# Kernel optimization log

Measured on AMD Instinct MI355X. Metric: run time of the kernel, lower is better.

The kernel has to match this reference:

```python
import jax, jax.numpy as jnp
import numpy as np

NEG_INF = -1e9

def setup_inputs() -> dict:
    key = jax.random.key(0)
    ks = jax.random.split(key, 6)
    B, M, RNN, H, D = 64, 1024, 1024, 512, 2048
    return {
        "h": jax.random.normal(ks[0], (B, RNN), dtype=jnp.float32),
        "att_feats": jax.random.normal(ks[1], (B, M, D), dtype=jnp.float32),
        "att_mask": jax.random.randint(ks[2], (B, M), 0, 2, dtype=jnp.int32),
        "p_att_feats": jax.random.normal(ks[3], (B, M, H), dtype=jnp.float32),
        "W_ah": jax.random.normal(ks[4], (H, RNN), dtype=jnp.float32) * (1.0 / np.sqrt(RNN)),
        "w_alpha": jax.random.normal(ks[5], (H,), dtype=jnp.float32) * (1.0 / np.sqrt(H)),
    }

def reference(h, att_feats, att_mask, p_att_feats, W_ah, w_alpha):
    # Wah(h): [B, H]
    wah = h @ W_ah.T
    # additive attention energies: tanh(Wah(h)[:, None, :] + p_att_feats) -> [B, M, H]
    e = jnp.tanh(wah[:, None, :] + p_att_feats)
    # project to scalar per region: [B, M]
    logits = jnp.einsum("bmh,h->bm", e, w_alpha)
    logits = jnp.where(att_mask == 0, NEG_INF, logits)
    alpha = jax.nn.softmax(logits, axis=-1)
    # weighted sum of region features: [B, D]
    att = jnp.einsum("bm,bmd->bd", alpha, att_feats)
    return att
```

## Files before the change

### kernel.cpp

```cpp
#include <hip/hip_runtime.h>
#include <math.h>

#define B   64
#define M   1024
#define RNN 1024
#define H   512
#define D   2048
#define NEG_INF -1e9f

__device__ __forceinline__ float fast_tanh(float x) {
    float ax = fabsf(x);
    float t  = __expf(-2.0f * ax);
    float r  = (1.0f - t) * __builtin_amdgcn_rcpf(1.0f + t);
    return copysignf(r, x);
}

__global__ __launch_bounds__(256) void k_wah(const float* __restrict__ h,
                                             const float* __restrict__ W,
                                             float* __restrict__ wah) {
    int wid  = (blockIdx.x * 256 + threadIdx.x) >> 6;
    int lane = threadIdx.x & 63;
    int b = wid >> 9;
    int j = wid & (H - 1);
    const float4* hp = (const float4*)(h + (size_t)b * RNN);
    const float4* wp = (const float4*)(W + (size_t)j * RNN);
    float acc = 0.0f;
#pragma unroll
    for (int t = 0; t < 4; ++t) {
        int i = lane + t * 64;
        float4 a = hp[i];
        float4 w = wp[i];
        acc += a.x * w.x + a.y * w.y + a.z * w.z + a.w * w.w;
    }
#pragma unroll
    for (int off = 32; off > 0; off >>= 1)
        acc += __shfl_down(acc, off);
    if (lane == 0) wah[wid] = acc;
}

__global__ __launch_bounds__(256) void k_logits(const float* __restrict__ wah,
                                                const float* __restrict__ p_att,
                                                const int* __restrict__ mask,
                                                const float* __restrict__ w_alpha,
                                                float* __restrict__ logits) {
    int row  = (blockIdx.x * 256 + threadIdx.x) >> 6;
    int lane = threadIdx.x & 63;
    int b = row >> 10;
    if (mask[row] == 0) {
        if (lane == 0) logits[row] = NEG_INF;
        return;
    }
    const float4* pp  = (const float4*)(p_att + (size_t)row * H);
    const float4* whp = (const float4*)(wah + (size_t)b * H);
    const float4* wap = (const float4*)w_alpha;
    float acc = 0.0f;
#pragma unroll
    for (int t = 0; t < 2; ++t) {
        int i = lane + t * 64;
        float4 p  = pp[i];
        float4 wh = whp[i];
        float4 wa = wap[i];
        acc += fast_tanh(p.x + wh.x) * wa.x;
        acc += fast_tanh(p.y + wh.y) * wa.y;
        acc += fast_tanh(p.z + wh.z) * wa.z;
        acc += fast_tanh(p.w + wh.w) * wa.w;
    }
#pragma unroll
    for (int off = 32; off > 0; off >>= 1)
        acc += __shfl_down(acc, off);
    if (lane == 0) logits[row] = acc;
}

__global__ __launch_bounds__(256) void k_prep(const float* __restrict__ logits,
                                              uint2* __restrict__ ent,
                                              int* __restrict__ cnt) {
    const int b = blockIdx.x, tid = threadIdx.x;
    const int lane = tid & 63, wid = tid >> 6;
    __shared__ float s_al[M];
    __shared__ float s_red[4];
    __shared__ int   s_wcnt[16];
    __shared__ int   s_base[17];

    const float4* lg = (const float4*)(logits + (size_t)b * M);
    float4 v = lg[tid];
    float mx = fmaxf(fmaxf(v.x, v.y), fmaxf(v.z, v.w));
#pragma unroll
    for (int off = 32; off > 0; off >>= 1)
        mx = fmaxf(mx, __shfl_xor(mx, off));
    if (lane == 0) s_red[wid] = mx;
    __syncthreads();
    mx = fmaxf(fmaxf(s_red[0], s_red[1]), fmaxf(s_red[2], s_red[3]));

    float e0 = __expf(v.x - mx), e1 = __expf(v.y - mx);
    float e2 = __expf(v.z - mx), e3 = __expf(v.w - mx);
    float se = e0 + e1 + e2 + e3;
#pragma unroll
    for (int off = 32; off > 0; off >>= 1)
        se += __shfl_xor(se, off);
    __syncthreads();
    if (lane == 0) s_red[wid] = se;
    __syncthreads();
    const float inv = 1.0f / (s_red[0] + s_red[1] + s_red[2] + s_red[3]);

    float4 av = {e0 * inv, e1 * inv, e2 * inv, e3 * inv};
    ((float4*)s_al)[tid] = av;
    __syncthreads();

#pragma unroll
    for (int p = 0; p < 4; ++p) {
        float a = s_al[p * 256 + tid];
        unsigned long long bal = __ballot(a != 0.0f);
        if (lane == 0) s_wcnt[p * 4 + wid] = __popcll(bal);
    }
    __syncthreads();
    if (tid == 0) {
        int run = 0;
#pragma unroll
        for (int i = 0; i < 16; ++i) { s_base[i] = run; run += s_wcnt[i]; }
        s_base[16] = run;
        cnt[b] = (run + 15) & ~15;
    }
    __syncthreads();

    uint2* eb = ent + (size_t)b * M;
#pragma unroll
    for (int p = 0; p < 4; ++p) {
        int m = p * 256 + tid;
        float a = s_al[m];
        unsigned long long bal = __ballot(a != 0.0f);
        int pos = __popcll(bal & ((1ull << lane) - 1ull));
        if (a != 0.0f)
            eb[s_base[p * 4 + wid] + pos] =
                make_uint2((unsigned)(m * D * 4), __float_as_uint(a));
    }
    int total = s_base[16];
    int padded = (total + 15) & ~15;
    if (tid < 16 && total + tid < padded)
        eb[total + tid] = make_uint2(0u, 0u);
}

__global__ __launch_bounds__(128) void k_att(const uint2* __restrict__ ent,
                                             const int* __restrict__ cnt,
                                             const float* __restrict__ feats,
                                             float* __restrict__ out) {
    const int b = blockIdx.x, dq = blockIdx.y;
    const int tid = threadIdx.x;
    const int d0 = dq * 512 + tid * 4;
    const char* fbase = (const char*)(feats + (size_t)b * M * D + d0);
    const uint2* eb = ent + (size_t)b * M;
    const int n = cnt[b];

    float4 acc[4];
#pragma unroll
    for (int c = 0; c < 4; ++c) acc[c] = make_float4(0.f, 0.f, 0.f, 0.f);

    for (int i = 0; i < n; i += 16) {
        uint2 e[16];
#pragma unroll
        for (int u = 0; u < 16; ++u) e[u] = eb[i + u];
        float4 f[16];
#pragma unroll
        for (int u = 0; u < 16; ++u)
            f[u] = *(const float4*)(fbase + e[u].x);
#pragma unroll
        for (int u = 0; u < 16; ++u) {
            float a = __uint_as_float(e[u].y);
            float4 F = f[u];
            int c = u & 3;
            acc[c].x += a * F.x; acc[c].y += a * F.y;
            acc[c].z += a * F.z; acc[c].w += a * F.w;
        }
    }
    float4 r;
    r.x = (acc[0].x + acc[1].x) + (acc[2].x + acc[3].x);
    r.y = (acc[0].y + acc[1].y) + (acc[2].y + acc[3].y);
    r.z = (acc[0].z + acc[1].z) + (acc[2].z + acc[3].z);
    r.w = (acc[0].w + acc[1].w) + (acc[2].w + acc[3].w);
    *(float4*)(out + (size_t)b * D + d0) = r;
}

extern "C" void kernel_launch(void* const* d_in, const int* in_sizes, int n_in,
                              void* d_out, int out_size, void* d_ws, size_t ws_size,
                              hipStream_t stream) {
    const float* h       = (const float*)d_in[0];
    const float* feats   = (const float*)d_in[1];
    const int*   mask    = (const int*)d_in[2];
    const float* p_att   = (const float*)d_in[3];
    const float* W_ah    = (const float*)d_in[4];
    const float* w_alpha = (const float*)d_in[5];
    float* out = (float*)d_out;

    float* ws     = (float*)d_ws;
    float* wah    = ws;
    float* logits = wah + B * H;
    uint2* ent    = (uint2*)(logits + B * M);
    int*   cnt    = (int*)(ent + B * M);

    k_wah   <<<dim3(B * H / 4), 256, 0, stream>>>(h, W_ah, wah);
    k_logits<<<dim3(B * M / 4), 256, 0, stream>>>(wah, p_att, mask, w_alpha, logits);
    k_prep  <<<dim3(B), 256, 0, stream>>>(logits, ent, cnt);
    k_att   <<<dim3(B, 4), 128, 0, stream>>>(ent, cnt, feats, out);
}
```

Baseline: 89.94 us.

## Split attention weighted sum across region chunks with separate reduction kernel

The weighted sum over attention features now splits the nonzero-region list into 8 chunks per batch, giving 1024 blocks instead of 256 so more of the GPU is busy. Entry lists are padded to a multiple of 64 and staged in shared memory. Each block writes partial sums to workspace, and a new reduce kernel adds the 8 partials. This costs an extra launch and extra partial-buffer traffic in exchange for more memory-level parallelism on the feature read.

```diff
diff --git a/kernel.cpp b/kernel.cpp
--- a/kernel.cpp
+++ b/kernel.cpp
@@ -7,6 +7,9 @@
 #define H   512
 #define D   2048
 #define NEG_INF -1e9f
+
+#define NCHUNK 8
+#define MAXCHUNK 128
 
 __device__ __forceinline__ float fast_tanh(float x) {
     float ax = fabsf(x);
@@ -118,7 +121,7 @@
 #pragma unroll
         for (int i = 0; i < 16; ++i) { s_base[i] = run; run += s_wcnt[i]; }
         s_base[16] = run;
-        cnt[b] = (run + 15) & ~15;
+        cnt[b] = (run + 63) & ~63;
     }
     __syncthreads();
 
@@ -134,41 +137,49 @@
                 make_uint2((unsigned)(m * D * 4), __float_as_uint(a));
     }
     int total = s_base[16];
-    int padded = (total + 15) & ~15;
-    if (tid < 16 && total + tid < padded)
+    int padded = (total + 63) & ~63;
+    if (tid < padded - total)
         eb[total + tid] = make_uint2(0u, 0u);
 }
 
-__global__ __launch_bounds__(128) void k_att(const uint2* __restrict__ ent,
-                                             const int* __restrict__ cnt,
-                                             const float* __restrict__ feats,
-                                             float* __restrict__ out) {
-    const int b = blockIdx.x, dq = blockIdx.y;
-    const int tid = threadIdx.x;
-    const int d0 = dq * 512 + tid * 4;
+__global__ __launch_bounds__(256) void k_att_partial(const uint2* __restrict__ ent,
+                                                     const int* __restrict__ cnt,
+                                                     const float* __restrict__ feats,
+                                                     float* __restrict__ partial) {
+    const int b    = blockIdx.x;
+    const int dblk = blockIdx.y;
+    const int c    = blockIdx.z;
+    const int tid  = threadIdx.x;
+
+    const int padded = cnt[b];
+    const int chunk  = padded >> 3;
+    const uint2* eb  = ent + (size_t)b * M + (size_t)c * chunk;
+
+    __shared__ uint2 s_ent[MAXCHUNK];
+    if (tid < chunk) s_ent[tid] = eb[tid];
+    __syncthreads();
+
+    const int d0 = dblk * 1024 + tid * 4;
     const char* fbase = (const char*)(feats + (size_t)b * M * D + d0);
-    const uint2* eb = ent + (size_t)b * M;
-    const int n = cnt[b];
 
     float4 acc[4];
 #pragma unroll
-    for (int c = 0; c < 4; ++c) acc[c] = make_float4(0.f, 0.f, 0.f, 0.f);
-
-    for (int i = 0; i < n; i += 16) {
-        uint2 e[16];
-#pragma unroll
-        for (int u = 0; u < 16; ++u) e[u] = eb[i + u];
-        float4 f[16];
-#pragma unroll
-        for (int u = 0; u < 16; ++u)
+    for (int q = 0; q < 4; ++q) acc[q] = make_float4(0.f, 0.f, 0.f, 0.f);
+
+    for (int i = 0; i < chunk; i += 8) {
+        uint2 e[8];
+#pragma unroll
+        for (int u = 0; u < 8; ++u) e[u] = s_ent[i + u];
+        float4 f[8];
+#pragma unroll
+        for (int u = 0; u < 8; ++u)
             f[u] = *(const float4*)(fbase + e[u].x);
 #pragma unroll
-        for (int u = 0; u < 16; ++u) {
+        for (int u = 0; u < 8; ++u) {
             float a = __uint_as_float(e[u].y);
-            float4 F = f[u];
-            int c = u & 3;
-            acc[c].x += a * F.x; acc[c].y += a * F.y;
-            acc[c].z += a * F.z; acc[c].w += a * F.w;
+            int q = u & 3;
+            acc[q].x += a * f[u].x; acc[q].y += a * f[u].y;
+            acc[q].z += a * f[u].z; acc[q].w += a * f[u].w;
         }
     }
     float4 r;
@@ -176,7 +187,20 @@
     r.y = (acc[0].y + acc[1].y) + (acc[2].y + acc[3].y);
     r.z = (acc[0].z + acc[1].z) + (acc[2].z + acc[3].z);
     r.w = (acc[0].w + acc[1].w) + (acc[2].w + acc[3].w);
-    *(float4*)(out + (size_t)b * D + d0) = r;
+    *(float4*)(partial + (((size_t)c * B + b) * D) + d0) = r;
+}
+
+__global__ __launch_bounds__(256) void k_att_reduce(const float* __restrict__ partial,
+                                                    float* __restrict__ out) {
+    int i4 = blockIdx.x * 256 + threadIdx.x;
+    const float4* p = (const float4*)partial;
+    float4 s = p[i4];
+#pragma unroll
+    for (int c = 1; c < NCHUNK; ++c) {
+        float4 v = p[(size_t)c * (B * D / 4) + i4];
+        s.x += v.x; s.y += v.y; s.z += v.z; s.w += v.w;
+    }
+    ((float4*)out)[i4] = s;
 }
 
 extern "C" void kernel_launch(void* const* d_in, const int* in_sizes, int n_in,
@@ -190,14 +214,16 @@
     const float* w_alpha = (const float*)d_in[5];
     float* out = (float*)d_out;
 
-    float* ws     = (float*)d_ws;
-    float* wah    = ws;
-    float* logits = wah + B * H;
-    uint2* ent    = (uint2*)(logits + B * M);
-    int*   cnt    = (int*)(ent + B * M);
-
-    k_wah   <<<dim3(B * H / 4), 256, 0, stream>>>(h, W_ah, wah);
-    k_logits<<<dim3(B * M / 4), 256, 0, stream>>>(wah, p_att, mask, w_alpha, logits);
-    k_prep  <<<dim3(B), 256, 0, stream>>>(logits, ent, cnt);
-    k_att   <<<dim3(B, 4), 128, 0, stream>>>(ent, cnt, feats, out);
-}
+    float* ws      = (float*)d_ws;
+    float* wah     = ws;
+    float* logits  = wah + B * H;
+    uint2* ent     = (uint2*)(logits + B * M);
+    int*   cnt     = (int*)(ent + B * M);
+    float* partial = (float*)(cnt + 64);
+
+    k_wah        <<<dim3(B * H / 4), 256, 0, stream>>>(h, W_ah, wah);
+    k_logits     <<<dim3(B * M / 4), 256, 0, stream>>>(wah, p_att, mask, w_alpha, logits);
+    k_prep       <<<dim3(B), 256, 0, stream>>>(logits, ent, cnt);
+    k_att_partial<<<dim3(B, D / 1024, NCHUNK), 256, 0, stream>>>(ent, cnt, feats, partial);
+    k_att_reduce <<<dim3(B * D / 1024), 256, 0, stream>>>(partial, out);
+}
```

After: 85.27 us. 5.2% less time.
